# Performance work log

Measured on AMD Instinct MI355X. Metric: run time of the kernel, lower is better.

## Reference

```python
import jax, jax.numpy as jnp
import numpy as np

N = 128       # SSM state size
L = 32768     # l_max / sequence length
DT_MIN, DT_MAX = 0.001, 0.1


def setup_inputs() -> dict:
    key = jax.random.key(0)
    ku, ka, kb, kc, ks = jax.random.split(key, 5)
    u = jax.random.normal(ku, (L,), dtype=jnp.float32)
    # lecun_normal: std = 1/sqrt(fan_in); shift A by -2I for stability over L powers
    A = jax.random.normal(ka, (N, N), dtype=jnp.float32) * (1.0 / np.sqrt(N)) - 2.0 * jnp.eye(N, dtype=jnp.float32)
    B = jax.random.normal(kb, (N, 1), dtype=jnp.float32)            # fan_in=1 -> std 1
    C = jax.random.normal(kc, (1, N), dtype=jnp.float32) * (1.0 / np.sqrt(N))
    D = jnp.ones((1,), dtype=jnp.float32)
    log_step = jax.random.uniform(ks, (1,), dtype=jnp.float32) * (np.log(DT_MAX) - np.log(DT_MIN)) + np.log(DT_MIN)
    return {"u": u, "A": A, "B": B, "C": C, "D": D, "log_step": log_step}


def discretize(a, b, step):
    # bilinear (Tustin) discretization, identical to the flax module
    i = jnp.eye(a.shape[0], dtype=a.dtype)
    bl = jnp.linalg.inv(i - (step / 2.0) * a)
    ab = bl @ (i + (step / 2.0) * a)
    bb = (bl * step) @ b
    return ab, bb


def k_conv(ab, bb, cb, l):
    # K[t] = cb @ ab^t @ bb  -- same math as the matrix_power list-comp,
    # computed with a single scan carrying x_t = ab^t @ bb  (N,1)
    def step(x, _):
        k_t = (cb @ x).reshape(())
        return ab @ x, k_t
    _, k = jax.lax.scan(step, bb, None, length=l)
    return k  # (l,)


def causal_convolution(u, k):
    l = u.shape[0]
    ud = jnp.fft.rfft(jnp.pad(u, (0, k.shape[0])))
    kd = jnp.fft.rfft(jnp.pad(k, (0, l)))
    return jnp.fft.irfft(ud * kd)[:l]


def reference(u, A, B, C, D, log_step):
    step = jnp.exp(log_step)
    ab, bb = discretize(A, B, step)
    K = k_conv(ab, bb, C, u.shape[0])
    return causal_convolution(u, K) + D * u
```

## Files before the change

### kernel.cpp

```cpp
#include <hip/hip_runtime.h>
#include <math.h>

#define L_SEQ 32768
#define SMD 132

typedef float f32x4 __attribute__((ext_vector_type(4)));
typedef short bf16x8 __attribute__((ext_vector_type(8)));

__device__ __forceinline__ unsigned short f2bf(float x) {
  unsigned u = __float_as_uint(x);
  u = u + 0x7FFFu + ((u >> 16) & 1u);
  return (unsigned short)(u >> 16);
}
__device__ __forceinline__ float bf2f(unsigned short h) {
  return __uint_as_float(((unsigned)h) << 16);
}
__device__ __forceinline__ unsigned packhl(float v) {
  unsigned short h = f2bf(v);
  unsigned short l = f2bf(v - bf2f(h));
  return ((unsigned)l << 16) | (unsigned)h;
}
__device__ __forceinline__ float unpackhl(unsigned d) {
  return bf2f((unsigned short)d) + bf2f((unsigned short)(d >> 16));
}
__device__ __forceinline__ bf16x8 exHi(uint4 q0, uint4 q1) {
  union { unsigned d[4]; bf16x8 v; } u;
  u.d[0] = (q0.y << 16) | (q0.x & 0xffffu);
  u.d[1] = (q0.w << 16) | (q0.z & 0xffffu);
  u.d[2] = (q1.y << 16) | (q1.x & 0xffffu);
  u.d[3] = (q1.w << 16) | (q1.z & 0xffffu);
  return u.v;
}
__device__ __forceinline__ bf16x8 exLo(uint4 q0, uint4 q1) {
  union { unsigned d[4]; bf16x8 v; } u;
  u.d[0] = (q0.y & 0xffff0000u) | (q0.x >> 16);
  u.d[1] = (q0.w & 0xffff0000u) | (q0.z >> 16);
  u.d[2] = (q1.y & 0xffff0000u) | (q1.x >> 16);
  u.d[3] = (q1.w & 0xffff0000u) | (q1.z >> 16);
  return u.v;
}

template<int ASRC, int BSRC, int OUT, int MODE>
__device__ void mm(unsigned* Ml, unsigned* Bt,
                   const unsigned* gA, const unsigned* gB,
                   unsigned* gO, int obase, int ldo,
                   int Mrows, int N, float c3) {
  const int t = threadIdx.x;
  const int lane = t & 63;
  const int la = lane & 15, g = lane >> 4;
  const int r0 = (t >> 6) << 5;
  const int fcn = (N + 15) >> 4;
  const bool act = (r0 < Mrows);
  __syncthreads();
  f32x4 acc[2][8];
#pragma unroll
  for (int a = 0; a < 2; ++a)
#pragma unroll
    for (int b = 0; b < 8; ++b) acc[a][b] = (f32x4){0.f, 0.f, 0.f, 0.f};
  if (act) {
#pragma unroll
    for (int kb = 0; kb < 4; ++kb) {
      const int k0 = (kb << 5) + (g << 3);
      bf16x8 Ah[2], Al[2];
#pragma unroll
      for (int fr = 0; fr < 2; ++fr) {
        int ar = r0 + (fr << 4) + la;
        uint4 q0 = make_uint4(0, 0, 0, 0), q1 = q0;
        if (ASRC == 0) {
          const uint4* p = (const uint4*)(Ml + ar * SMD + k0);
          q0 = p[0]; q1 = p[1];
        } else if (ar < Mrows) {
          const uint4* p = (const uint4*)(gA + ar * 128 + k0);
          q0 = p[0]; q1 = p[1];
        }
        Ah[fr] = exHi(q0, q1);
        Al[fr] = exLo(q0, q1);
      }
#pragma unroll
      for (int fc = 0; fc < 8; ++fc) if (fc < fcn) {
        int c = (fc << 4) + la;
        uint4 q0 = make_uint4(0, 0, 0, 0), q1 = q0;
        if (BSRC == 0) {
          const uint4* p = (const uint4*)(Bt + c * SMD + k0);
          q0 = p[0]; q1 = p[1];
        } else if (c < N) {
          const uint4* p = (const uint4*)(gB + c * 128 + k0);
          q0 = p[0]; q1 = p[1];
        }
        bf16x8 Bh = exHi(q0, q1), Bl = exLo(q0, q1);
#pragma unroll
        for (int fr = 0; fr < 2; ++fr) if (r0 + (fr << 4) < Mrows) {
          acc[fr][fc] = __builtin_amdgcn_mfma_f32_16x16x32_bf16(Ah[fr], Bh, acc[fr][fc], 0, 0, 0);
          acc[fr][fc] = __builtin_amdgcn_mfma_f32_16x16x32_bf16(Ah[fr], Bl, acc[fr][fc], 0, 0, 0);
          acc[fr][fc] = __builtin_amdgcn_mfma_f32_16x16x32_bf16(Al[fr], Bh, acc[fr][fc], 0, 0, 0);
        }
      }
    }
  }
  __syncthreads();
  if (act) {
#pragma unroll
    for (int fr = 0; fr < 2; ++fr) if (r0 + (fr << 4) < Mrows)
#pragma unroll
      for (int fc = 0; fc < 8; ++fc) if (fc < fcn) {
        int rbase = r0 + (fr << 4) + (g << 2);
        int cc = (fc << 4) + la;
        unsigned dw[4];
#pragma unroll
        for (int j = 0; j < 4; ++j) {
          int rr = rbase + j;
          float v = acc[fr][fc][j];
          if (MODE == 2)
            v += unpackhl(Ml[rr * SMD + cc]) + unpackhl(Bt[cc * SMD + rr]) +
                 ((rr == cc) ? 1.f : 0.f);
          if (MODE == 3) v = c3 * v - ((rr == cc) ? 1.f : 0.f);
          dw[j] = packhl(v);
        }
        if (OUT == 0) {
#pragma unroll
          for (int j = 0; j < 4; ++j) Ml[(rbase + j) * SMD + cc] = dw[j];
        } else if (OUT == 1) {
          if (cc < N)
            *(uint4*)(gO + (obase + cc) * ldo + rbase) =
                make_uint4(dw[0], dw[1], dw[2], dw[3]);
        } else {
#pragma unroll
          for (int j = 0; j < 4; ++j)
            if (rbase + j < Mrows) gO[(obase + rbase + j) * 128 + cc] = dw[j];
        }
      }
  }
}

__device__ __forceinline__ void transposeMB(const unsigned* Ml, unsigned* Bt) {
  __syncthreads();
  const int t = threadIdx.x;
  const int c = t & 127;
  const int kb = (t >> 7) << 6;
#pragma unroll
  for (int k = 0; k < 64; ++k)
    Bt[c * SMD + kb + k] = Ml[(kb + k) * SMD + c];
}

__global__ void __launch_bounds__(256, 1) chain2(const float* __restrict__ A,
                                                 const float* __restrict__ Bv,
                                                 const float* __restrict__ Cv,
                                                 const float* __restrict__ lstep,
                                                 unsigned* wsdw) {
  extern __shared__ unsigned lds[];
  unsigned* Ml = lds;
  unsigned* Bt = lds + 128 * SMD;
  unsigned* gU12t = wsdw + blockIdx.x * (128 * SMD);
  unsigned* Rt = wsdw + 2 * 128 * SMD;
  unsigned* S  = Rt + 256 * 128;

  const int t = threadIdx.x;
  const float step = expf(lstep[0]);
  const float alpha = 0.5f * step / (1.0f + step);
  const float c3 = 2.f / (1.f + step);

#pragma unroll
  for (int i = 0; i < 64; ++i) {
    int idx = t + (i << 8);
    int r = idx >> 7, c = idx & 127;
    float d = (r == c) ? 1.f : 0.f;
    unsigned pk = packhl(alpha * (A[idx] + 2.f * d));
    Ml[r * SMD + c] = pk;
    Bt[c * SMD + r] = pk;
  }

  mm<0,0,0,0>(Ml, Bt, 0, 0, 0, 0, 0, 128, 128, 0.f);
  mm<0,0,1,2>(Ml, Bt, 0, 0, gU12t, 0, SMD, 128, 128, 0.f);
  transposeMB(Ml, Bt);
  mm<0,0,0,0>(Ml, Bt, 0, 0, 0, 0, 0, 128, 128, 0.f);
  transposeMB(Ml, Bt);
  mm<0,0,0,0>(Ml, Bt, 0, 0, 0, 0, 0, 128, 128, 0.f);
  mm<0,0,0,2>(Ml, Bt, 0, 0, 0, 0, 0, 128, 128, 0.f);
  __syncthreads();
  {
    const uint4* src = (const uint4*)gU12t;
    uint4* dst4 = (uint4*)Bt;
    for (int i = t; i < (128 * SMD) / 4; i += 256) dst4[i] = src[i];
  }
  mm<0,0,0,3>(Ml, Bt, 0, 0, 0, 0, 0, 128, 128, c3);

  if (blockIdx.x == 0) {
    __syncthreads();
    if (t < 128) {
      float a2 = 0.f;
      for (int k = 0; k < 128; ++k) a2 = fmaf(unpackhl(Ml[t * SMD + k]), Bv[k], a2);
      Rt[t] = packhl(0.5f * step * (a2 + Bv[t]));
    }
    for (int k = 0; k < 8; ++k) {
      mm<0,1,1,0>(Ml, Bt, 0, Rt, Rt, 1 << k, 128, 128, 1 << k, 0.f);
      if (k < 7) {
        transposeMB(Ml, Bt);
        mm<0,0,0,0>(Ml, Bt, 0, 0, 0, 0, 0, 128, 128, 0.f);
      }
    }
  } else {
    __syncthreads();
    if (t < 128) S[t] = packhl(Cv[t]);
    for (int k = 0; k < 8; ++k) {
      transposeMB(Ml, Bt);
      mm<0,0,0,0>(Ml, Bt, 0, 0, 0, 0, 0, 128, 128, 0.f);
    }
    for (int k = 0; k < 7; ++k) {
      transposeMB(Ml, Bt);
      mm<1,0,2,0>(Ml, Bt, S, 0, S, 1 << k, 0, 1 << k, 128, 0.f);
      if (k < 6)
        mm<0,0,0,0>(Ml, Bt, 0, 0, 0, 0, 0, 128, 128, 0.f);
    }
  }
}

__global__ __launch_bounds__(256) void kmat_k(const unsigned* __restrict__ Sdw,
                                              const unsigned* __restrict__ Rtdw,
                                              float* __restrict__ Kv) {
  __shared__ float srow[128];
  int t1 = blockIdx.x, t0 = threadIdx.x;
  if (t0 < 128) srow[t0] = unpackhl(Sdw[t1 * 128 + t0]);
  __syncthreads();
  const unsigned* rr = Rtdw + t0 * 128;
  float acc = 0.f;
#pragma unroll 8
  for (int k = 0; k < 128; k += 4) {
    uint4 q = *(const uint4*)(rr + k);
    acc = fmaf(srow[k],     unpackhl(q.x), acc);
    acc = fmaf(srow[k + 1], unpackhl(q.y), acc);
    acc = fmaf(srow[k + 2], unpackhl(q.z), acc);
    acc = fmaf(srow[k + 3], unpackhl(q.w), acc);
  }
  Kv[t1 * 256 + t0] = acc;
}

__global__ __launch_bounds__(256) void conv_k(const float* __restrict__ u,
                                              const float* __restrict__ Kv,
                                              float* __restrict__ Pp) {
  __shared__ __align__(16) float ks[1024];
  __shared__ __align__(16) float usw[2048];

  int bid = blockIdx.x, tid = threadIdx.x;
  int m = 0;
  while ((m + 1) * (m + 2) / 2 <= bid) m++;
  int c = bid - m * (m + 1) / 2;
  int w0 = (m - c - 1) << 10;

  for (int idx = tid; idx < 1024; idx += 256) ks[idx] = Kv[(c << 10) + idx];
  for (int idx = tid; idx < 2048; idx += 256) {
    int gi = w0 + idx;
    float v = (gi >= 0) ? u[gi] : 0.f;
    int b = idx >> 2;
    int pb = b ^ ((b >> 3) & 7);
    usw[(pb << 2) | (idx & 3)] = v;
  }
  __syncthreads();

  int tb = tid << 2;

#define LD4(x)                                                      \
  (*(const float4*)&usw[((((x) >> 2) ^ ((((x) >> 2) >> 3) & 7)) << 2)])

  float4 wlo = LD4(1020 + tb);
  float4 whi = LD4(1024 + tb);
  float acc0 = 0.f, acc1 = 0.f, acc2 = 0.f, acc3 = 0.f;

#pragma unroll 4
  for (int s8 = 0; s8 < 1024; s8 += 4) {
    float4 k4 = *(const float4*)&ks[s8];
    acc0 = fmaf(k4.x, whi.x, acc0);
    acc0 = fmaf(k4.y, wlo.w, acc0);
    acc0 = fmaf(k4.z, wlo.z, acc0);
    acc0 = fmaf(k4.w, wlo.y, acc0);
    acc1 = fmaf(k4.x, whi.y, acc1);
    acc1 = fmaf(k4.y, whi.x, acc1);
    acc1 = fmaf(k4.z, wlo.w, acc1);
    acc1 = fmaf(k4.w, wlo.z, acc1);
    acc2 = fmaf(k4.x, whi.z, acc2);
    acc2 = fmaf(k4.y, whi.y, acc2);
    acc2 = fmaf(k4.z, whi.x, acc2);
    acc2 = fmaf(k4.w, wlo.w, acc2);
    acc3 = fmaf(k4.x, whi.w, acc3);
    acc3 = fmaf(k4.y, whi.z, acc3);
    acc3 = fmaf(k4.z, whi.y, acc3);
    acc3 = fmaf(k4.w, whi.x, acc3);
    if (s8 < 1020) {
      whi = wlo;
      wlo = LD4(1016 + tb - s8);
    }
  }
#undef LD4

  float* dst = Pp + (c << 15) + (m << 10) + tb;
  *(float4*)dst = make_float4(acc0, acc1, acc2, acc3);
}

__global__ __launch_bounds__(256) void reduce_k(const float* __restrict__ Pp,
                                                const float* __restrict__ u,
                                                const float* __restrict__ D,
                                                float* __restrict__ y) {
  int t = blockIdx.x * 256 + threadIdx.x;
  if (t >= L_SEQ) return;
  int mm_ = t >> 10;
  float acc = D[0] * u[t];
  for (int c = 0; c <= mm_; ++c) acc += Pp[(c << 15) + t];
  y[t] = acc;
}

extern "C" void kernel_launch(void* const* d_in, const int* in_sizes, int n_in,
                              void* d_out, int out_size, void* d_ws, size_t ws_size,
                              hipStream_t stream) {
  (void)in_sizes; (void)n_in; (void)out_size; (void)ws_size;
  const float* u     = (const float*)d_in[0];
  const float* A     = (const float*)d_in[1];
  const float* B     = (const float*)d_in[2];
  const float* C     = (const float*)d_in[3];
  const float* D     = (const float*)d_in[4];
  const float* lstep = (const float*)d_in[5];
  float* y = (float*)d_out;
  unsigned* wsdw = (unsigned*)d_ws;
  float* wsf = (float*)d_ws;

  unsigned* Rt = wsdw + 33792;
  unsigned* S  = wsdw + 66560;
  float* Kv = wsf + 82944;
  float* Pp = wsf + 115712;

  (void)hipFuncSetAttribute((const void*)chain2,
                            hipFuncAttributeMaxDynamicSharedMemorySize, 135168);
  hipLaunchKernelGGL(chain2, dim3(2), dim3(256), 135168, stream, A, B, C, lstep, wsdw);
  hipLaunchKernelGGL(kmat_k, dim3(128), dim3(256), 0, stream, S, Rt, Kv);
  hipLaunchKernelGGL(conv_k, dim3(528), dim3(256), 0, stream, u, Kv, Pp);
  hipLaunchKernelGGL(reduce_k, dim3(128), dim3(256), 0, stream, Pp, u, D, y);
}
```

Before: 259.3 us.

## Restructure matrix-power chain with split hi/lo planes and 1024-thread 2D wave tiling

Rewrites the serial matrix-power chain kernel to keep the bf16 hi and lo parts in separate LDS planes with a swizzled k-ordering, so MFMA operands load directly without per-element unpacking. The block grows from 256 to 1024 threads with a 4x4 wave tiling of 32x32 output tiles. Each multiply also produces the transposed product in the same pass, which removes the explicit LDS transposes between squarings. The goal is to shorten the latency-bound chain of dependent 128x128 multiplies that run on only two blocks. The cost is duplicated MFMA work for the transposed outputs and more intricate swizzle indexing, which raises correctness risk.

```diff
diff --git a/kernel.cpp b/kernel.cpp
--- a/kernel.cpp
+++ b/kernel.cpp
@@ -2,234 +2,302 @@
 #include <math.h>
 
 #define L_SEQ 32768
-#define SMD 132
-
+#define RSTR 136
+#define PL   17408
+#define GP   16384
+
+typedef unsigned short u16;
 typedef float f32x4 __attribute__((ext_vector_type(4)));
 typedef short bf16x8 __attribute__((ext_vector_type(8)));
-
-__device__ __forceinline__ unsigned short f2bf(float x) {
+typedef u16 u16x4 __attribute__((ext_vector_type(4)));
+
+__device__ __forceinline__ u16 f2bf(float x) {
   unsigned u = __float_as_uint(x);
   u = u + 0x7FFFu + ((u >> 16) & 1u);
-  return (unsigned short)(u >> 16);
-}
-__device__ __forceinline__ float bf2f(unsigned short h) {
+  return (u16)(u >> 16);
+}
+__device__ __forceinline__ float bf2f(u16 h) {
   return __uint_as_float(((unsigned)h) << 16);
 }
-__device__ __forceinline__ unsigned packhl(float v) {
-  unsigned short h = f2bf(v);
-  unsigned short l = f2bf(v - bf2f(h));
-  return ((unsigned)l << 16) | (unsigned)h;
-}
-__device__ __forceinline__ float unpackhl(unsigned d) {
-  return bf2f((unsigned short)d) + bf2f((unsigned short)(d >> 16));
-}
-__device__ __forceinline__ bf16x8 exHi(uint4 q0, uint4 q1) {
-  union { unsigned d[4]; bf16x8 v; } u;
-  u.d[0] = (q0.y << 16) | (q0.x & 0xffffu);
-  u.d[1] = (q0.w << 16) | (q0.z & 0xffffu);
-  u.d[2] = (q1.y << 16) | (q1.x & 0xffffu);
-  u.d[3] = (q1.w << 16) | (q1.z & 0xffffu);
-  return u.v;
-}
-__device__ __forceinline__ bf16x8 exLo(uint4 q0, uint4 q1) {
-  union { unsigned d[4]; bf16x8 v; } u;
-  u.d[0] = (q0.y & 0xffff0000u) | (q0.x >> 16);
-  u.d[1] = (q0.w & 0xffff0000u) | (q0.z >> 16);
-  u.d[2] = (q1.y & 0xffff0000u) | (q1.x >> 16);
-  u.d[3] = (q1.w & 0xffff0000u) | (q1.z >> 16);
-  return u.v;
-}
-
-template<int ASRC, int BSRC, int OUT, int MODE>
-__device__ void mm(unsigned* Ml, unsigned* Bt,
-                   const unsigned* gA, const unsigned* gB,
-                   unsigned* gO, int obase, int ldo,
-                   int Mrows, int N, float c3) {
-  const int t = threadIdx.x;
-  const int lane = t & 63;
+__device__ __forceinline__ int sg(int k) {
+  return (k & 7) + ((k >> 5) << 3) + (((k >> 3) & 3) << 5);
+}
+__device__ __forceinline__ f32x4 MF(bf16x8 a, bf16x8 b, f32x4 c) {
+  return __builtin_amdgcn_mfma_f32_16x16x32_bf16(a, b, c, 0, 0, 0);
+}
+
+template<int ASRC,int BSRC,int OUTM,int OUTG,int MODE>
+__device__ void mm(u16* lds, const u16* gA, int aPl, const u16* gB, int bPl,
+                   u16* gO, int oPl, int gOrow0, u16* gO2,
+                   int Mrows, int N, float c3, const u16* gE, const u16* gEt) {
+  u16* Mh = lds;          u16* Ml = lds + PL;
+  u16* Th = lds + 2 * PL; u16* Tl = lds + 3 * PL;
+  const int t = threadIdx.x, lane = t & 63;
   const int la = lane & 15, g = lane >> 4;
-  const int r0 = (t >> 6) << 5;
-  const int fcn = (N + 15) >> 4;
-  const bool act = (r0 < Mrows);
+  const int w = t >> 6;
+  const int r0 = (w >> 2) << 5, c0 = (w & 3) << 5;
+  constexpr bool doA = (OUTM == 2) || (OUTG == 2) || (OUTG == 3);
+  constexpr bool doT = (OUTM >= 1) || (OUTG == 1) || (OUTG == 3);
+  const bool act = (r0 < Mrows) && (c0 < N);
+
   __syncthreads();
-  f32x4 acc[2][8];
-#pragma unroll
-  for (int a = 0; a < 2; ++a)
-#pragma unroll
-    for (int b = 0; b < 8; ++b) acc[a][b] = (f32x4){0.f, 0.f, 0.f, 0.f};
+
+  f32x4 acc[2][2], accT[2][2];
+#pragma unroll
+  for (int i = 0; i < 2; ++i)
+#pragma unroll
+    for (int j = 0; j < 2; ++j) {
+      acc[i][j] = (f32x4){0.f, 0.f, 0.f, 0.f};
+      accT[i][j] = (f32x4){0.f, 0.f, 0.f, 0.f};
+    }
+
   if (act) {
 #pragma unroll
     for (int kb = 0; kb < 4; ++kb) {
-      const int k0 = (kb << 5) + (g << 3);
-      bf16x8 Ah[2], Al[2];
+      const int kp = (g << 5) + (kb << 3);
+      bf16x8 Ah[2], Al[2], Bh[2], Bl[2];
 #pragma unroll
       for (int fr = 0; fr < 2; ++fr) {
-        int ar = r0 + (fr << 4) + la;
-        uint4 q0 = make_uint4(0, 0, 0, 0), q1 = q0;
-        if (ASRC == 0) {
-          const uint4* p = (const uint4*)(Ml + ar * SMD + k0);
-          q0 = p[0]; q1 = p[1];
-        } else if (ar < Mrows) {
-          const uint4* p = (const uint4*)(gA + ar * 128 + k0);
-          q0 = p[0]; q1 = p[1];
-        }
-        Ah[fr] = exHi(q0, q1);
-        Al[fr] = exLo(q0, q1);
+        const int ar = r0 + (fr << 4) + la;
+        if constexpr (ASRC == 0) {
+          Ah[fr] = *(const bf16x8*)(Mh + ar * RSTR + kp);
+          Al[fr] = *(const bf16x8*)(Ml + ar * RSTR + kp);
+        } else {
+          Ah[fr] = *(const bf16x8*)(gA + ar * 128 + kp);
+          Al[fr] = *(const bf16x8*)(gA + aPl + ar * 128 + kp);
+        }
       }
 #pragma unroll
-      for (int fc = 0; fc < 8; ++fc) if (fc < fcn) {
-        int c = (fc << 4) + la;
-        uint4 q0 = make_uint4(0, 0, 0, 0), q1 = q0;
-        if (BSRC == 0) {
-          const uint4* p = (const uint4*)(Bt + c * SMD + k0);
-          q0 = p[0]; q1 = p[1];
-        } else if (c < N) {
-          const uint4* p = (const uint4*)(gB + c * 128 + k0);
-          q0 = p[0]; q1 = p[1];
-        }
-        bf16x8 Bh = exHi(q0, q1), Bl = exLo(q0, q1);
-#pragma unroll
-        for (int fr = 0; fr < 2; ++fr) if (r0 + (fr << 4) < Mrows) {
-          acc[fr][fc] = __builtin_amdgcn_mfma_f32_16x16x32_bf16(Ah[fr], Bh, acc[fr][fc], 0, 0, 0);
-          acc[fr][fc] = __builtin_amdgcn_mfma_f32_16x16x32_bf16(Ah[fr], Bl, acc[fr][fc], 0, 0, 0);
-          acc[fr][fc] = __builtin_amdgcn_mfma_f32_16x16x32_bf16(Al[fr], Bh, acc[fr][fc], 0, 0, 0);
+      for (int fc = 0; fc < 2; ++fc) {
+        const int bc = c0 + (fc << 4) + la;
+        if constexpr (BSRC == 0) {
+          Bh[fc] = *(const bf16x8*)(Th + bc * RSTR + kp);
+          Bl[fc] = *(const bf16x8*)(Tl + bc * RSTR + kp);
+        } else {
+          Bh[fc] = *(const bf16x8*)(gB + bc * 128 + kp);
+          Bl[fc] = *(const bf16x8*)(gB + bPl + bc * 128 + kp);
         }
       }
-    }
-  }
+#pragma unroll
+      for (int fr = 0; fr < 2; ++fr)
+#pragma unroll
+        for (int fc = 0; fc < 2; ++fc) {
+          if constexpr (doA) {
+            acc[fr][fc] = MF(Ah[fr], Bh[fc], acc[fr][fc]);
+            acc[fr][fc] = MF(Ah[fr], Bl[fc], acc[fr][fc]);
+            acc[fr][fc] = MF(Al[fr], Bh[fc], acc[fr][fc]);
+          }
+          if constexpr (doT) {
+            accT[fr][fc] = MF(Bh[fc], Ah[fr], accT[fr][fc]);
+            accT[fr][fc] = MF(Bh[fc], Al[fr], accT[fr][fc]);
+            accT[fr][fc] = MF(Bl[fc], Ah[fr], accT[fr][fc]);
+          }
+        }
+    }
+  }
+
   __syncthreads();
-  if (act) {
-#pragma unroll
-    for (int fr = 0; fr < 2; ++fr) if (r0 + (fr << 4) < Mrows)
-#pragma unroll
-      for (int fc = 0; fc < 8; ++fc) if (fc < fcn) {
-        int rbase = r0 + (fr << 4) + (g << 2);
-        int cc = (fc << 4) + la;
-        unsigned dw[4];
+
+  if (!act) return;
+
+  if constexpr (doT) {
+#pragma unroll
+    for (int fr = 0; fr < 2; ++fr)
+#pragma unroll
+      for (int fc = 0; fc < 2; ++fc) {
+        const int rr = r0 + (fr << 4) + la;
+        const int cb = c0 + (fc << 4) + (g << 2);
+        const int scb = sg(cb);
+        float v[4];
+#pragma unroll
+        for (int j = 0; j < 4; ++j) v[j] = accT[fr][fc][j];
+        if constexpr (MODE == 2) {
+#pragma unroll
+          for (int j = 0; j < 4; ++j)
+            v[j] += bf2f(gE[rr * 128 + scb + j]) + bf2f(gE[GP + rr * 128 + scb + j])
+                  + bf2f(Mh[rr * RSTR + scb + j]) + bf2f(Ml[rr * RSTR + scb + j])
+                  + ((rr == cb + j) ? 1.f : 0.f);
+        }
+        if constexpr (MODE == 4) {
+#pragma unroll
+          for (int j = 0; j < 4; ++j)
+            v[j] = c3 * (v[j] + bf2f(gE[rr * 128 + scb + j]) +
+                         bf2f(gE[GP + rr * 128 + scb + j])) -
+                   ((rr == cb + j) ? 1.f : 0.f);
+        }
+        u16x4 hi, lo;
 #pragma unroll
         for (int j = 0; j < 4; ++j) {
-          int rr = rbase + j;
-          float v = acc[fr][fc][j];
-          if (MODE == 2)
-            v += unpackhl(Ml[rr * SMD + cc]) + unpackhl(Bt[cc * SMD + rr]) +
-                 ((rr == cc) ? 1.f : 0.f);
-          if (MODE == 3) v = c3 * v - ((rr == cc) ? 1.f : 0.f);
-          dw[j] = packhl(v);
-        }
-        if (OUT == 0) {
-#pragma unroll
-          for (int j = 0; j < 4; ++j) Ml[(rbase + j) * SMD + cc] = dw[j];
-        } else if (OUT == 1) {
-          if (cc < N)
-            *(uint4*)(gO + (obase + cc) * ldo + rbase) =
-                make_uint4(dw[0], dw[1], dw[2], dw[3]);
-        } else {
+          u16 h = f2bf(v[j]); hi[j] = h; lo[j] = f2bf(v[j] - bf2f(h));
+        }
+        if constexpr (OUTM == 2) {
+          *(u16x4*)(Mh + rr * RSTR + scb) = hi;
+          *(u16x4*)(Ml + rr * RSTR + scb) = lo;
+        }
+        if constexpr (OUTG == 1) {
+          if (rr < Mrows) {
+            *(u16x4*)(gO + (gOrow0 + rr) * 128 + scb) = hi;
+            *(u16x4*)(gO + oPl + (gOrow0 + rr) * 128 + scb) = lo;
+          }
+        }
+        if constexpr (OUTG == 3) {
+          *(u16x4*)(gO + rr * 128 + scb) = hi;
+          *(u16x4*)(gO + oPl + rr * 128 + scb) = lo;
+        }
+      }
+  }
+  if constexpr (doA) {
+#pragma unroll
+    for (int fr = 0; fr < 2; ++fr)
+#pragma unroll
+      for (int fc = 0; fc < 2; ++fc) {
+        const int cc = c0 + (fc << 4) + la;
+        const int rb = r0 + (fr << 4) + (g << 2);
+        const int srb = sg(rb);
+        float v[4];
+#pragma unroll
+        for (int j = 0; j < 4; ++j) v[j] = acc[fr][fc][j];
+        if constexpr (MODE == 2) {
+          const int scc = sg(cc);
 #pragma unroll
           for (int j = 0; j < 4; ++j)
-            if (rbase + j < Mrows) gO[(obase + rbase + j) * 128 + cc] = dw[j];
+            v[j] += bf2f(gE[(rb + j) * 128 + scc]) + bf2f(gE[GP + (rb + j) * 128 + scc])
+                  + bf2f(Th[cc * RSTR + srb + j]) + bf2f(Tl[cc * RSTR + srb + j])
+                  + ((rb + j == cc) ? 1.f : 0.f);
+        }
+        if constexpr (MODE == 4) {
+#pragma unroll
+          for (int j = 0; j < 4; ++j)
+            v[j] = c3 * (v[j] + bf2f(gEt[cc * 128 + srb + j]) +
+                         bf2f(gEt[GP + cc * 128 + srb + j])) -
+                   ((rb + j == cc) ? 1.f : 0.f);
+        }
+        u16x4 hi, lo;
+#pragma unroll
+        for (int j = 0; j < 4; ++j) {
+          u16 h = f2bf(v[j]); hi[j] = h; lo[j] = f2bf(v[j] - bf2f(h));
+        }
+        if constexpr (OUTM == 2) {
+          *(u16x4*)(Th + cc * RSTR + srb) = hi;
+          *(u16x4*)(Tl + cc * RSTR + srb) = lo;
+        }
+        if constexpr (OUTG == 2) {
+          if (cc < N) {
+            *(u16x4*)(gO + (gOrow0 + cc) * 128 + srb) = hi;
+            *(u16x4*)(gO + oPl + (gOrow0 + cc) * 128 + srb) = lo;
+          }
+        }
+        if constexpr (OUTG == 3) {
+          *(u16x4*)(gO2 + cc * 128 + srb) = hi;
+          *(u16x4*)(gO2 + oPl + cc * 128 + srb) = lo;
         }
       }
   }
 }
 
-__device__ __forceinline__ void transposeMB(const unsigned* Ml, unsigned* Bt) {
-  __syncthreads();
-  const int t = threadIdx.x;
-  const int c = t & 127;
-  const int kb = (t >> 7) << 6;
-#pragma unroll
-  for (int k = 0; k < 64; ++k)
-    Bt[c * SMD + kb + k] = Ml[(kb + k) * SMD + c];
-}
-
-__global__ void __launch_bounds__(256, 1) chain2(const float* __restrict__ A,
-                                                 const float* __restrict__ Bv,
-                                                 const float* __restrict__ Cv,
-                                                 const float* __restrict__ lstep,
-                                                 unsigned* wsdw) {
-  extern __shared__ unsigned lds[];
-  unsigned* Ml = lds;
-  unsigned* Bt = lds + 128 * SMD;
-  unsigned* gU12t = wsdw + blockIdx.x * (128 * SMD);
-  unsigned* Rt = wsdw + 2 * 128 * SMD;
-  unsigned* S  = Rt + 256 * 128;
+__global__ void __launch_bounds__(1024) chain_k(const float* __restrict__ A,
+                                                const float* __restrict__ Bv,
+                                                const float* __restrict__ Cv,
+                                                const float* __restrict__ lstep,
+                                                u16* ws) {
+  extern __shared__ u16 lds[];
+  const int bid = blockIdx.x;
+  u16* gT    = ws + bid * 131072;
+  u16* gU12  = gT + 32768;
+  u16* gU12t = gT + 65536;
+  u16* rt = ws + 262144;
+  u16* gs = ws + 327680;
 
   const int t = threadIdx.x;
   const float step = expf(lstep[0]);
-  const float alpha = 0.5f * step / (1.0f + step);
+  const float alpha = 0.5f * step / (1.f + step);
   const float c3 = 2.f / (1.f + step);
-
-#pragma unroll
-  for (int i = 0; i < 64; ++i) {
-    int idx = t + (i << 8);
-    int r = idx >> 7, c = idx & 127;
-    float d = (r == c) ? 1.f : 0.f;
-    unsigned pk = packhl(alpha * (A[idx] + 2.f * d));
-    Ml[r * SMD + c] = pk;
-    Bt[c * SMD + r] = pk;
-  }
-
-  mm<0,0,0,0>(Ml, Bt, 0, 0, 0, 0, 0, 128, 128, 0.f);
-  mm<0,0,1,2>(Ml, Bt, 0, 0, gU12t, 0, SMD, 128, 128, 0.f);
-  transposeMB(Ml, Bt);
-  mm<0,0,0,0>(Ml, Bt, 0, 0, 0, 0, 0, 128, 128, 0.f);
-  transposeMB(Ml, Bt);
-  mm<0,0,0,0>(Ml, Bt, 0, 0, 0, 0, 0, 128, 128, 0.f);
-  mm<0,0,0,2>(Ml, Bt, 0, 0, 0, 0, 0, 128, 128, 0.f);
-  __syncthreads();
-  {
-    const uint4* src = (const uint4*)gU12t;
-    uint4* dst4 = (uint4*)Bt;
-    for (int i = t; i < (128 * SMD) / 4; i += 256) dst4[i] = src[i];
-  }
-  mm<0,0,0,3>(Ml, Bt, 0, 0, 0, 0, 0, 128, 128, c3);
-
-  if (blockIdx.x == 0) {
+  u16* Mh = lds; u16* Ml = lds + PL; u16* Th = lds + 2 * PL; u16* Tl = lds + 3 * PL;
+
+#pragma unroll
+  for (int i = 0; i < 4; ++i) {
+    int e4 = (t + (i << 10)) << 2;
+    int r = e4 >> 7, c = e4 & 127;
+    float4 av = *(const float4*)(A + e4);
+    float vv[4] = {av.x, av.y, av.z, av.w};
+    u16x4 hi, lo;
+#pragma unroll
+    for (int j = 0; j < 4; ++j) {
+      float v = alpha * (vv[j] + ((r == c + j) ? 2.f : 0.f));
+      u16 h = f2bf(v); hi[j] = h; lo[j] = f2bf(v - bf2f(h));
+    }
+    int sc = sg(c), sr = sg(r);
+    *(u16x4*)(Mh + r * RSTR + sc) = hi;
+    *(u16x4*)(Ml + r * RSTR + sc) = lo;
+    *(u16x4*)(gT + r * 128 + sc) = hi;
+    *(u16x4*)(gT + GP + r * 128 + sc) = lo;
+#pragma unroll
+    for (int j = 0; j < 4; ++j) {
+      Th[(c + j) * RSTR + sr] = hi[j];
+      Tl[(c + j) * RSTR + sr] = lo[j];
+    }
+  }
+
+  mm<0,0,2,0,0>(lds, 0,0, 0,0, 0,0,0,0, 128,128, 0.f, 0,0);
+  mm<1,0,0,3,2>(lds, gT,GP, 0,0, gU12,GP,0,gU12t, 128,128, 0.f, gT,0);
+  mm<0,0,2,0,0>(lds, 0,0, 0,0, 0,0,0,0, 128,128, 0.f, 0,0);
+  mm<1,0,2,0,4>(lds, gU12,GP, 0,0, 0,0,0,0, 128,128, c3, gU12,gU12t);
+
+  if (bid == 0) {
     __syncthreads();
     if (t < 128) {
       float a2 = 0.f;
-      for (int k = 0; k < 128; ++k) a2 = fmaf(unpackhl(Ml[t * SMD + k]), Bv[k], a2);
-      Rt[t] = packhl(0.5f * step * (a2 + Bv[t]));
+      for (int p = 0; p < 128; ++p)
+        a2 = fmaf(bf2f(Mh[t * RSTR + p]) + bf2f(Ml[t * RSTR + p]), Bv[sg(p)], a2);
+      float v = 0.5f * step * (a2 + Bv[t]);
+      u16 h = f2bf(v);
+      rt[sg(t)] = h;
+      rt[32768 + sg(t)] = f2bf(v - bf2f(h));
     }
     for (int k = 0; k < 8; ++k) {
-      mm<0,1,1,0>(Ml, Bt, 0, Rt, Rt, 1 << k, 128, 128, 1 << k, 0.f);
-      if (k < 7) {
-        transposeMB(Ml, Bt);
-        mm<0,0,0,0>(Ml, Bt, 0, 0, 0, 0, 0, 128, 128, 0.f);
-      }
+      mm<0,1,0,2,0>(lds, 0,0, rt,32768, rt,32768,(1<<k),0, 128,(1<<k), 0.f, 0,0);
+      if (k < 7) mm<0,0,2,0,0>(lds, 0,0, 0,0, 0,0,0,0, 128,128, 0.f, 0,0);
     }
   } else {
     __syncthreads();
-    if (t < 128) S[t] = packhl(Cv[t]);
-    for (int k = 0; k < 8; ++k) {
-      transposeMB(Ml, Bt);
-      mm<0,0,0,0>(Ml, Bt, 0, 0, 0, 0, 0, 128, 128, 0.f);
-    }
+    if (t < 128) {
+      float v = Cv[t];
+      u16 h = f2bf(v);
+      gs[sg(t)] = h;
+      gs[GP + sg(t)] = f2bf(v - bf2f(h));
+    }
+    for (int k = 0; k < 8; ++k)
+      mm<0,0,2,0,0>(lds, 0,0, 0,0, 0,0,0,0, 128,128, 0.f, 0,0);
     for (int k = 0; k < 7; ++k) {
-      transposeMB(Ml, Bt);
-      mm<1,0,2,0>(Ml, Bt, S, 0, S, 1 << k, 0, 1 << k, 128, 0.f);
-      if (k < 6)
-        mm<0,0,0,0>(Ml, Bt, 0, 0, 0, 0, 0, 128, 128, 0.f);
-    }
-  }
-}
-
-__global__ __launch_bounds__(256) void kmat_k(const unsigned* __restrict__ Sdw,
-                                              const unsigned* __restrict__ Rtdw,
+      mm<1,0,0,1,0>(lds, gs,GP, 0,0, gs,GP,(1<<k),0, (1<<k),128, 0.f, 0,0);
+      if (k < 6) mm<0,0,2,0,0>(lds, 0,0, 0,0, 0,0,0,0, 128,128, 0.f, 0,0);
+    }
+  }
+}
+
+__global__ __launch_bounds__(256) void kmat_k(const u16* __restrict__ gs,
+                                              const u16* __restrict__ rt,
                                               float* __restrict__ Kv) {
   __shared__ float srow[128];
   int t1 = blockIdx.x, t0 = threadIdx.x;
-  if (t0 < 128) srow[t0] = unpackhl(Sdw[t1 * 128 + t0]);
+  if (t0 < 128)
+    srow[t0] = bf2f(gs[t1 * 128 + t0]) + bf2f(gs[GP + t1 * 128 + t0]);
   __syncthreads();
-  const unsigned* rr = Rtdw + t0 * 128;
+  const u16* rh = rt + t0 * 128;
+  const u16* rl = rt + 32768 + t0 * 128;
   float acc = 0.f;
-#pragma unroll 8
-  for (int k = 0; k < 128; k += 4) {
-    uint4 q = *(const uint4*)(rr + k);
-    acc = fmaf(srow[k],     unpackhl(q.x), acc);
-    acc = fmaf(srow[k + 1], unpackhl(q.y), acc);
-    acc = fmaf(srow[k + 2], unpackhl(q.z), acc);
-    acc = fmaf(srow[k + 3], unpackhl(q.w), acc);
+#pragma unroll 4
+  for (int p = 0; p < 128; p += 8) {
+    uint4 qh = *(const uint4*)(rh + p);
+    uint4 ql = *(const uint4*)(rl + p);
+    unsigned dh[4] = {qh.x, qh.y, qh.z, qh.w};
+    unsigned dl[4] = {ql.x, ql.y, ql.z, ql.w};
+#pragma unroll
+    for (int j = 0; j < 4; ++j) {
+      acc = fmaf(srow[p + 2 * j],     bf2f((u16)dh[j]) + bf2f((u16)dl[j]), acc);
+      acc = fmaf(srow[p + 2 * j + 1],
+                 bf2f((u16)(dh[j] >> 16)) + bf2f((u16)(dl[j] >> 16)), acc);
+    }
   }
   Kv[t1 * 256 + t0] = acc;
 }
@@ -318,18 +386,17 @@
   const float* D     = (const float*)d_in[4];
   const float* lstep = (const float*)d_in[5];
   float* y = (float*)d_out;
-  unsigned* wsdw = (unsigned*)d_ws;
-  float* wsf = (float*)d_ws;
-
-  unsigned* Rt = wsdw + 33792;
-  unsigned* S  = wsdw + 66560;
-  float* Kv = wsf + 82944;
-  float* Pp = wsf + 115712;
-
-  (void)hipFuncSetAttribute((const void*)chain2,
-                            hipFuncAttributeMaxDynamicSharedMemorySize, 135168);
-  hipLaunchKernelGGL(chain2, dim3(2), dim3(256), 135168, stream, A, B, C, lstep, wsdw);
-  hipLaunchKernelGGL(kmat_k, dim3(128), dim3(256), 0, stream, S, Rt, Kv);
+  u16* ws = (u16*)d_ws;
+
+  u16* rt = ws + 262144;
+  u16* gs = ws + 327680;
+  float* Kv = (float*)((char*)d_ws + 720896);
+  float* Pp = Kv + 32768;
+
+  (void)hipFuncSetAttribute((const void*)chain_k,
+                            hipFuncAttributeMaxDynamicSharedMemorySize, 139264);
+  hipLaunchKernelGGL(chain_k, dim3(2), dim3(1024), 139264, stream, A, B, C, lstep, ws);
+  hipLaunchKernelGGL(kmat_k, dim3(128), dim3(256), 0, stream, gs, rt, Kv);
   hipLaunchKernelGGL(conv_k, dim3(528), dim3(256), 0, stream, u, Kv, Pp);
   hipLaunchKernelGGL(reduce_k, dim3(128), dim3(256), 0, stream, Pp, u, D, y);
 }
```

Result: faster. 214.9 us (-17.1%).
